# Kernel optimization log

Hardware: AMD Instinct MI355X
Metric: run time of the kernel (lower is better)

Reference implementation:

```python
import jax, jax.numpy as jnp
import numpy as np
import math

# hyperparams matching init_kwargs
GAMMA_S = 0.8
GAMMA_U = 0.8
RHO_I = 0.1
RHO_T = 0.1
EPS = 1e-10
TAU_MIN = 0.005
TAU_MAX = 1.0
TAU_INIT = 0.07
GRAD_CLIP = 5.0
ETA_INIT = 0.01
ETA_MIN = 0.0001
N_STATE = 2900000
BSZ = 4096
DIM = 1024


def setup_inputs() -> dict:
    key = jax.random.key(0)
    k1, k2 = jax.random.split(key)
    imf = jax.random.normal(k1, (BSZ, DIM), jnp.float32)
    imf = imf / jnp.linalg.norm(imf, axis=1, keepdims=True)
    txf = jax.random.normal(k2, (BSZ, DIM), jnp.float32)
    txf = txf / jnp.linalg.norm(txf, axis=1, keepdims=True)
    return {
        "image_features": imf,
        "text_features": txf,
        "s_I": jnp.zeros((N_STATE,), jnp.float32),
        "s_T": jnp.zeros((N_STATE,), jnp.float32),
        "tau_I": jnp.full((N_STATE,), TAU_INIT, jnp.float32),
        "tau_T": jnp.full((N_STATE,), TAU_INIT, jnp.float32),
        "u_I": jnp.zeros((N_STATE,), jnp.float32),
        "u_T": jnp.zeros((N_STATE,), jnp.float32),
        "b_I": jnp.zeros((N_STATE,), jnp.float32),
        "b_T": jnp.zeros((N_STATE,), jnp.float32),
        "image_ids": jnp.arange(BSZ, dtype=jnp.int32),
        "text_ids": jnp.arange(BSZ, dtype=jnp.int32),
        "epoch": 5,
        "max_epoch": 30,
    }


def reference(image_features, text_features, s_I, s_T, tau_I, tau_T,
              u_I, u_T, b_I, b_T, image_ids, text_ids, epoch, max_epoch):
    B = image_features.shape[0]
    sim = jnp.einsum('id,jd->ij', image_features, text_features)  # [B,B]
    diag_sim = jnp.diagonal(sim)                                  # [B]

    tau_image = tau_I[image_ids]  # [B]
    tau_text = tau_T[text_ids]    # [B]

    image_diffs = sim - diag_sim[:, None]
    text_diffs = sim - diag_sim[None, :]
    # .detach() in torch -> stop_gradient
    idt = jax.lax.stop_gradient(image_diffs / tau_image[:, None])
    tdt = jax.lax.stop_gradient(text_diffs / tau_text[None, :])

    # max-trick state b_I / b_T: running row/col max per sample id
    old_b_I = b_I[image_ids]
    new_b_I = jnp.maximum(jnp.max(idt, axis=1), old_b_I)  # [B]
    old_b_T = b_T[text_ids]
    new_b_T = jnp.maximum(jnp.max(tdt, axis=0), old_b_T)  # [B]

    exp_image_diffs = jnp.exp(idt - new_b_I[:, None])
    exp_text_diffs = jnp.exp(tdt - new_b_T[None, :])
    g_I = jnp.sum(exp_image_diffs, axis=1, keepdims=True) / (B - 1)  # [B,1]
    g_T = jnp.sum(exp_text_diffs, axis=0, keepdims=True) / (B - 1)   # [1,B]

    # moving-average s state (compute_last=False, last_g_* = None path)
    s_I_new = (1.0 - GAMMA_S) * s_I[image_ids] * jnp.exp(old_b_I - new_b_I) + GAMMA_S * g_I[:, 0]
    s_T_new = (1.0 - GAMMA_S) * s_T[text_ids] * jnp.exp(old_b_T - new_b_T) + GAMMA_S * g_T[0, :]
    s_I_b = s_I_new[:, None]  # same shape as g_I
    s_T_b = s_T_new[None, :]  # same shape as g_T

    weights_image = exp_image_diffs / (s_I_b + EPS)
    weights_text = exp_text_diffs / (s_T_b + EPS)

    image_loss = jnp.sum(weights_image * image_diffs, axis=1, keepdims=True) / (B - 1)
    text_loss = jnp.sum(weights_text * text_diffs, axis=0, keepdims=True) / (B - 1)
    total_loss = image_loss.mean() + text_loss.mean()

    grad_tau_image = (jnp.log(s_I_b) + new_b_I[:, None] + RHO_I
                      - jnp.sum(weights_image * idt, axis=1, keepdims=True) / (B - 1))
    grad_tau_text = (jnp.log(s_T_b) + new_b_T[None, :] + RHO_T
                     - jnp.sum(weights_text * tdt, axis=0, keepdims=True) / (B - 1))

    u_I_new = (1.0 - GAMMA_U) * u_I[image_ids] + GAMMA_U * jnp.clip(grad_tau_image[:, 0], -GRAD_CLIP, GRAD_CLIP)
    u_T_new = (1.0 - GAMMA_U) * u_T[text_ids] + GAMMA_U * jnp.clip(grad_tau_text[0, :], -GRAD_CLIP, GRAD_CLIP)

    eta_cur = ETA_MIN + (ETA_INIT - ETA_MIN) * math.cos(math.pi * (epoch / max_epoch) / 2)
    tau_I_new = jnp.clip(tau_image - eta_cur * u_I_new, TAU_MIN, TAU_MAX)
    tau_T_new = jnp.clip(tau_text - eta_cur * u_T_new, TAU_MIN, TAU_MAX)

    # scattered state writes (the module's in-place buffer updates)
    b_I_out = b_I.at[image_ids].set(new_b_I)
    b_T_out = b_T.at[text_ids].set(new_b_T)
    s_I_out = s_I.at[image_ids].set(s_I_new)
    s_T_out = s_T.at[text_ids].set(s_T_new)
    u_I_out = u_I.at[image_ids].set(u_I_new)
    u_T_out = u_T.at[text_ids].set(u_T_new)
    tau_I_out = tau_I.at[image_ids].set(tau_I_new)
    tau_T_out = tau_T.at[text_ids].set(tau_T_new)

    avg_image_tau = tau_image.mean()
    avg_text_tau = tau_text.mean()

    return (g_I, g_T, grad_tau_image, grad_tau_text, total_loss,
            avg_image_tau, avg_text_tau,
            s_I_out, s_T_out, u_I_out, u_T_out,
            b_I_out, b_T_out, tau_I_out, tau_T_out)
```

## Files before the change

kernel.cpp:

```cpp
#include <hip/hip_runtime.h>
#include <math.h>

#define BSZ 4096
#define DIM 1024
#define NST 2900000

constexpr float GAMMA_S   = 0.8f;
constexpr float GAMMA_U   = 0.8f;
constexpr float RHO_I_C   = 0.1f;
constexpr float RHO_T_C   = 0.1f;
constexpr float C_EPS     = 1e-10f;
constexpr float TAU_MIN_C = 0.005f;
constexpr float TAU_MAX_C = 1.0f;
constexpr float GCLIP     = 5.0f;
constexpr float ETA_INIT_C = 0.01f;
constexpr float ETA_MIN_C  = 1e-4f;
constexpr float PI_F       = 3.14159265358979323846f;

typedef __bf16 bf16x8 __attribute__((ext_vector_type(8)));
typedef float  f32x4  __attribute__((ext_vector_type(4)));

__device__ __forceinline__ unsigned short f2bf(float f) {
    unsigned int u = __float_as_uint(f);
    u += 0x7fffu + ((u >> 16) & 1u);
    return (unsigned short)(u >> 16);
}
__device__ __forceinline__ float bf2f(unsigned short s) {
    return __uint_as_float(((unsigned int)s) << 16);
}

__global__ __launch_bounds__(256) void conv_diag(const float* __restrict__ imf,
                                                 const float* __restrict__ txf,
                                                 unsigned short* __restrict__ abf,
                                                 unsigned short* __restrict__ bbf,
                                                 const float* __restrict__ tau_I,
                                                 const float* __restrict__ tau_T,
                                                 const float* __restrict__ b_I,
                                                 const float* __restrict__ b_T,
                                                 const int* __restrict__ iid,
                                                 const int* __restrict__ tid_,
                                                 float* diag, float* tauIg, float* tauTg,
                                                 float* obI, float* obT,
                                                 float* __restrict__ scal) {
    if (blockIdx.x == 0 && threadIdx.x < 3) scal[threadIdx.x] = 0.f;
    const int w  = threadIdx.x >> 6;
    const int ln = threadIdx.x & 63;
    const int i  = blockIdx.x * 4 + w;
    float dot = 0.f;
#pragma unroll
    for (int k = 0; k < 4; ++k) {
        const int off = i * DIM + k * 256 + ln * 4;
        float4 a = *(const float4*)&imf[off];
        float4 b = *(const float4*)&txf[off];
        ushort4 ra, rb;
        ra.x = f2bf(a.x); ra.y = f2bf(a.y); ra.z = f2bf(a.z); ra.w = f2bf(a.w);
        rb.x = f2bf(b.x); rb.y = f2bf(b.y); rb.z = f2bf(b.z); rb.w = f2bf(b.w);
        *(ushort4*)&abf[off] = ra;
        *(ushort4*)&bbf[off] = rb;
        dot += bf2f(ra.x) * bf2f(rb.x) + bf2f(ra.y) * bf2f(rb.y) +
               bf2f(ra.z) * bf2f(rb.z) + bf2f(ra.w) * bf2f(rb.w);
    }
#pragma unroll
    for (int m = 32; m; m >>= 1) dot += __shfl_xor(dot, m);
    if (ln == 0) {
        diag[i] = dot;
        const int id = iid[i];
        tauIg[i] = tau_I[id];
        obI[i]   = b_I[id];
        const int td = tid_[i];
        tauTg[i] = tau_T[td];
        obT[i]   = b_T[td];
    }
}

__device__ __forceinline__ void async16(const void* g, void* l) {
    __builtin_amdgcn_global_load_lds(
        (const __attribute__((address_space(1))) void*)g,
        (__attribute__((address_space(3))) void*)l, 16, 0, 0);
}

__global__ __launch_bounds__(256) void gemm_fused(const unsigned short* __restrict__ A,
                                                  const unsigned short* __restrict__ B,
                                                  const float* __restrict__ diag,
                                                  const float* __restrict__ tauIg,
                                                  const float* __restrict__ tauTg,
                                                  float* __restrict__ rpM,
                                                  float* __restrict__ rpE,
                                                  float* __restrict__ rpV,
                                                  float* __restrict__ cpM,
                                                  float* __restrict__ cpE,
                                                  float* __restrict__ cpV,
                                                  const float* __restrict__ s_I,
                                                  const float* __restrict__ s_T,
                                                  const float* __restrict__ u_I,
                                                  const float* __restrict__ u_T,
                                                  const float* __restrict__ b_I,
                                                  const float* __restrict__ b_T,
                                                  const float* __restrict__ tau_I,
                                                  const float* __restrict__ tau_T,
                                                  float* __restrict__ outbase) {
    __shared__ unsigned short As[128 * 32];
    __shared__ unsigned short Bs[128 * 32];

    const int tid = threadIdx.x;
    const int gid = ((blockIdx.x >> 4) << 3) | (blockIdx.x & 7);

    if ((blockIdx.x >> 3) & 1) {
        const size_t idx = (size_t)gid * 256 + tid;
        const size_t stride = (size_t)1024 * 256;
        const size_t NV = (NST - 1) / 4;
        const float* srcs[8] = {s_I, s_T, u_I, u_T, b_I, b_T, tau_I, tau_T};
#pragma unroll
        for (int a = 0; a < 8; ++a) {
            const float* s = srcs[a];
            float* d = outbase + (size_t)a * NST;
            for (size_t cidx = idx; cidx < NV; cidx += stride) {
                const size_t e = 1 + 4 * cidx;
                float4 v = make_float4(s[e], s[e + 1], s[e + 2], s[e + 3]);
                *(float4*)&d[e] = v;
            }
            if (idx == 0) d[0] = s[0];
            if (idx < 3)  d[NST - 3 + idx] = s[NST - 3 + idx];
        }
        return;
    }

    const int bjIdx = gid & 31, biIdx = gid >> 5;
    const int bi = biIdx * 128;
    const int bj = bjIdx * 128;
    const int lane = tid & 63;
    const int wave = tid >> 6;
    const int m_base = (wave >> 1) * 64;
    const int n_base = (wave & 1) * 64;

    const int c0 = tid, c1 = tid + 256;
    const int r0 = c0 >> 2, kg0 = ((c0 & 3) ^ ((r0 >> 1) & 3)) * 8;
    const int r1 = c1 >> 2, kg1 = ((c1 & 3) ^ ((r1 >> 1) & 3)) * 8;

    f32x4 acc[4][4];
#pragma unroll
    for (int m = 0; m < 4; ++m)
#pragma unroll
        for (int n = 0; n < 4; ++n)
            acc[m][n] = (f32x4){0.f, 0.f, 0.f, 0.f};

    const int mrow = lane & 15;
    const int q    = lane >> 4;

    for (int k0 = 0; k0 < DIM; k0 += 32) {
        __syncthreads();
        async16(&A[(size_t)(bi + r0) * DIM + k0 + kg0], &As[c0 * 8]);
        async16(&A[(size_t)(bi + r1) * DIM + k0 + kg1], &As[c1 * 8]);
        async16(&B[(size_t)(bj + r0) * DIM + k0 + kg0], &Bs[c0 * 8]);
        async16(&B[(size_t)(bj + r1) * DIM + k0 + kg1], &Bs[c1 * 8]);
        __syncthreads();

        bf16x8 af[4], bfr[4];
#pragma unroll
        for (int t = 0; t < 4; ++t) {
            const int rlA = m_base + t * 16 + mrow;
            const int rlB = n_base + t * 16 + mrow;
            af[t]  = *(const bf16x8*)&As[rlA * 32 + (q ^ ((rlA >> 1) & 3)) * 8];
            bfr[t] = *(const bf16x8*)&Bs[rlB * 32 + (q ^ ((rlB >> 1) & 3)) * 8];
        }
#pragma unroll
        for (int mt = 0; mt < 4; ++mt)
#pragma unroll
            for (int nt = 0; nt < 4; ++nt)
                acc[mt][nt] = __builtin_amdgcn_mfma_f32_16x16x32_bf16(
                    af[mt], bfr[nt], acc[mt][nt], 0, 0, 0);
    }

    __syncthreads();
    float* prm = (float*)Bs;
    if (tid < 128) {
        prm[tid]       = diag[bi + tid];
        prm[128 + tid] = 1.0f / tauIg[bi + tid];
        prm[256 + tid] = diag[bj + tid];
        prm[384 + tid] = 1.0f / tauTg[bj + tid];
    }
    __syncthreads();

    float* red = (float*)As;
    const int rowq = (lane >> 4) * 4;

#pragma unroll
    for (int mt = 0; mt < 4; ++mt)
#pragma unroll
        for (int r = 0; r < 4; ++r) {
            const int row_l = m_base + mt * 16 + rowq + r;
            const float dgr = prm[row_l];
            const float itr = prm[128 + row_l];
            float v0 = (acc[mt][0][r] - dgr) * itr;
            float v1 = (acc[mt][1][r] - dgr) * itr;
            float v2 = (acc[mt][2][r] - dgr) * itr;
            float v3 = (acc[mt][3][r] - dgr) * itr;
            float m = fmaxf(fmaxf(v0, v1), fmaxf(v2, v3));
#pragma unroll
            for (int x = 1; x <= 8; x <<= 1) m = fmaxf(m, __shfl_xor(m, x));
            const float e0 = __expf(v0 - m), e1 = __expf(v1 - m);
            const float e2 = __expf(v2 - m), e3 = __expf(v3 - m);
            float se = e0 + e1 + e2 + e3;
            float sv = e0 * v0 + e1 * v1 + e2 * v2 + e3 * v3;
#pragma unroll
            for (int x = 1; x <= 8; x <<= 1) {
                se += __shfl_xor(se, x);
                sv += __shfl_xor(sv, x);
            }
            if ((lane & 15) == 0) {
                const int idx = wave * 64 + mt * 16 + rowq + r;
                red[idx] = m; red[256 + idx] = se; red[512 + idx] = sv;
            }
        }

#pragma unroll
    for (int nt = 0; nt < 4; ++nt) {
        const int col_l = n_base + nt * 16 + (lane & 15);
        const float dgc = prm[256 + col_l];
        const float itc = prm[384 + col_l];
        float m = -INFINITY;
#pragma unroll
        for (int mt = 0; mt < 4; ++mt)
#pragma unroll
            for (int r = 0; r < 4; ++r)
                m = fmaxf(m, (acc[mt][nt][r] - dgc) * itc);
        m = fmaxf(m, __shfl_xor(m, 16));
        m = fmaxf(m, __shfl_xor(m, 32));
        float se = 0.f, sv = 0.f;
#pragma unroll
        for (int mt = 0; mt < 4; ++mt)
#pragma unroll
            for (int r = 0; r < 4; ++r) {
                const float v = (acc[mt][nt][r] - dgc) * itc;
                const float e = __expf(v - m);
                se += e; sv += e * v;
            }
        se += __shfl_xor(se, 16); se += __shfl_xor(se, 32);
        sv += __shfl_xor(sv, 16); sv += __shfl_xor(sv, 32);
        if (lane < 16) {
            const int idx = wave * 64 + nt * 16 + lane;
            red[768 + idx] = m; red[1024 + idx] = se; red[1280 + idx] = sv;
        }
    }
    __syncthreads();

    if (tid < 128) {
        const int rg = tid, li = rg & 63;
        const int w0 = (rg >> 6) * 2, w1 = w0 + 1;
        const float mA = red[w0 * 64 + li], mB = red[w1 * 64 + li];
        const float M = fmaxf(mA, mB);
        const float fA = __expf(mA - M), fB = __expf(mB - M);
        const size_t o = (size_t)bjIdx * BSZ + bi + rg;
        rpM[o] = M;
        rpE[o] = red[256 + w0 * 64 + li] * fA + red[256 + w1 * 64 + li] * fB;
        rpV[o] = red[512 + w0 * 64 + li] * fA + red[512 + w1 * 64 + li] * fB;
    } else {
        const int cg = tid - 128, li = cg & 63;
        const int w0 = cg >> 6, w1 = w0 + 2;
        const float mA = red[768 + w0 * 64 + li], mB = red[768 + w1 * 64 + li];
        const float M = fmaxf(mA, mB);
        const float fA = __expf(mA - M), fB = __expf(mB - M);
        const size_t o = (size_t)biIdx * BSZ + bj + cg;
        cpM[o] = M;
        cpE[o] = red[1024 + w0 * 64 + li] * fA + red[1024 + w1 * 64 + li] * fB;
        cpV[o] = red[1280 + w0 * 64 + li] * fA + red[1280 + w1 * 64 + li] * fB;
    }
}

__global__ __launch_bounds__(256) void finalize(const float* __restrict__ s_I,
                                                const float* __restrict__ s_T,
                                                const float* __restrict__ u_I,
                                                const float* __restrict__ u_T,
                                                const int* __restrict__ iid,
                                                const int* __restrict__ tid_,
                                                const int* __restrict__ epoch,
                                                const int* __restrict__ maxep,
                                                const float* __restrict__ tauIg,
                                                const float* __restrict__ tauTg,
                                                const float* __restrict__ obI,
                                                const float* __restrict__ obT,
                                                const float* __restrict__ rpM,
                                                const float* __restrict__ rpE,
                                                const float* __restrict__ rpV,
                                                const float* __restrict__ cpM,
                                                const float* __restrict__ cpE,
                                                const float* __restrict__ cpV,
                                                float* __restrict__ out) {
    const int i = blockIdx.x * 256 + threadIdx.x;

    const float eta = ETA_MIN_C + (ETA_INIT_C - ETA_MIN_C) *
                      cosf(0.5f * PI_F * ((float)epoch[0] / (float)maxep[0]));
    const float invBm1 = 1.0f / (float)(BSZ - 1);
    const float invB   = 1.0f / (float)BSZ;

    float* o_gI   = out;
    float* o_gT   = out + BSZ;
    float* o_gti  = out + 2 * BSZ;
    float* o_gtt  = out + 3 * BSZ;
    float* o_sI   = out + 4 * BSZ + 3;
    float* o_sT   = o_sI + NST;
    float* o_uI   = o_sT + NST;
    float* o_uT   = o_uI + NST;
    float* o_bI   = o_uT + NST;
    float* o_bT   = o_bI + NST;
    float* o_tauI = o_bT + NST;
    float* o_tauT = o_tauI + NST;

    float lossc, tI_B, tT_B;

    {
        const int id = iid[i];
        float mr = -INFINITY;
#pragma unroll
        for (int k = 0; k < 32; ++k) mr = fmaxf(mr, rpM[(size_t)k * BSZ + i]);
        const float tau = tauIg[i];
        const float ob = obI[i];
        const float nb = fmaxf(ob, mr);
        float se = 0.f, sv = 0.f;
#pragma unroll
        for (int k = 0; k < 32; ++k) {
            const float f = __expf(rpM[(size_t)k * BSZ + i] - nb);
            se += rpE[(size_t)k * BSZ + i] * f;
            sv += rpV[(size_t)k * BSZ + i] * f;
        }
        const float g = se * invBm1;
        const float s_new = (1.f - GAMMA_S) * s_I[id] * __expf(ob - nb) + GAMMA_S * g;
        const float W = sv * invBm1 / (s_new + C_EPS);
        const float grad = logf(s_new) + nb + RHO_I_C - W;
        lossc = tau * W;
        tI_B  = tau * invB;
        const float gc = fminf(fmaxf(grad, -GCLIP), GCLIP);
        const float u_new = (1.f - GAMMA_U) * u_I[id] + GAMMA_U * gc;
        const float tau_new = fminf(fmaxf(tau - eta * u_new, TAU_MIN_C), TAU_MAX_C);
        o_gI[i] = g;
        o_gti[i] = grad;
        o_sI[id] = s_new;
        o_uI[id] = u_new;
        o_bI[id] = nb;
        o_tauI[id] = tau_new;
    }
    {
        const int id = tid_[i];
        float mc = -INFINITY;
#pragma unroll
        for (int k = 0; k < 32; ++k) mc = fmaxf(mc, cpM[(size_t)k * BSZ + i]);
        const float tau = tauTg[i];
        const float ob = obT[i];
        const float nb = fmaxf(ob, mc);
        float se = 0.f, sv = 0.f;
#pragma unroll
        for (int k = 0; k < 32; ++k) {
            const float f = __expf(cpM[(size_t)k * BSZ + i] - nb);
            se += cpE[(size_t)k * BSZ + i] * f;
            sv += cpV[(size_t)k * BSZ + i] * f;
        }
        const float g = se * invBm1;
        const float s_new = (1.f - GAMMA_S) * s_T[id] * __expf(ob - nb) + GAMMA_S * g;
        const float W = sv * invBm1 / (s_new + C_EPS);
        const float grad = logf(s_new) + nb + RHO_T_C - W;
        lossc += tau * W;
        tT_B   = tau * invB;
        const float gc = fminf(fmaxf(grad, -GCLIP), GCLIP);
        const float u_new = (1.f - GAMMA_U) * u_T[id] + GAMMA_U * gc;
        const float tau_new = fminf(fmaxf(tau - eta * u_new, TAU_MIN_C), TAU_MAX_C);
        o_gT[i] = g;
        o_gtt[i] = grad;
        o_sT[id] = s_new;
        o_uT[id] = u_new;
        o_bT[id] = nb;
        o_tauT[id] = tau_new;
    }

    float v0 = lossc * invB, v1 = tI_B, v2 = tT_B;
#pragma unroll
    for (int o = 32; o; o >>= 1) {
        v0 += __shfl_down(v0, o);
        v1 += __shfl_down(v1, o);
        v2 += __shfl_down(v2, o);
    }
    __shared__ float lds[4][3];
    const int wv = threadIdx.x >> 6, ln = threadIdx.x & 63;
    if (ln == 0) { lds[wv][0] = v0; lds[wv][1] = v1; lds[wv][2] = v2; }
    __syncthreads();
    if (threadIdx.x == 0) {
        atomicAdd(&out[4 * BSZ + 0], lds[0][0] + lds[1][0] + lds[2][0] + lds[3][0]);
        atomicAdd(&out[4 * BSZ + 1], lds[0][1] + lds[1][1] + lds[2][1] + lds[3][1]);
        atomicAdd(&out[4 * BSZ + 2], lds[0][2] + lds[1][2] + lds[2][2] + lds[3][2]);
    }
}

extern "C" void kernel_launch(void* const* d_in, const int* in_sizes, int n_in,
                              void* d_out, int out_size, void* d_ws, size_t ws_size,
                              hipStream_t stream) {
    const float* imf   = (const float*)d_in[0];
    const float* txf   = (const float*)d_in[1];
    const float* s_I   = (const float*)d_in[2];
    const float* s_T   = (const float*)d_in[3];
    const float* tau_I = (const float*)d_in[4];
    const float* tau_T = (const float*)d_in[5];
    const float* u_I   = (const float*)d_in[6];
    const float* u_T   = (const float*)d_in[7];
    const float* b_I   = (const float*)d_in[8];
    const float* b_T   = (const float*)d_in[9];
    const int* iid     = (const int*)d_in[10];
    const int* tid_    = (const int*)d_in[11];
    const int* epoch   = (const int*)d_in[12];
    const int* maxep   = (const int*)d_in[13];

    float* out = (float*)d_out;
    float* ws  = (float*)d_ws;

    float* diag  = ws + 0 * BSZ;
    float* tauIg = ws + 1 * BSZ;
    float* tauTg = ws + 2 * BSZ;
    float* obI   = ws + 3 * BSZ;
    float* obT   = ws + 4 * BSZ;
    float* rpM   = ws + 5 * BSZ;
    float* rpE   = rpM + (size_t)32 * BSZ;
    float* rpV   = rpE + (size_t)32 * BSZ;
    float* cpM   = rpV + (size_t)32 * BSZ;
    float* cpE   = cpM + (size_t)32 * BSZ;
    float* cpV   = cpE + (size_t)32 * BSZ;
    unsigned short* abf = (unsigned short*)(cpV + (size_t)32 * BSZ);
    unsigned short* bbf = abf + (size_t)BSZ * DIM;

    conv_diag<<<BSZ / 4, 256, 0, stream>>>(imf, txf, abf, bbf, tau_I, tau_T, b_I, b_T,
                                           iid, tid_, diag, tauIg, tauTg, obI, obT,
                                           out + 4 * BSZ);
    gemm_fused<<<2048, 256, 0, stream>>>(abf, bbf, diag, tauIg, tauTg,
                                         rpM, rpE, rpV, cpM, cpE, cpV,
                                         s_I, s_T, u_I, u_T, b_I, b_T, tau_I, tau_T,
                                         out + 4 * BSZ + 3);
    finalize<<<BSZ / 256, 256, 0, stream>>>(s_I, s_T, u_I, u_T, iid, tid_, epoch, maxep,
                                            tauIg, tauTg, obI, obT,
                                            rpM, rpE, rpV, cpM, cpE, cpV, out);
}
```

Before: 283.4 us.

## Deepen GEMM K-tile to 64, vectorize state copy loads, parallelize finalize

The GEMM K-step grows from 32 to 64 with a new XOR swizzle over 8 chunks. This halves the number of barrier pairs per tile at the cost of doubled LDS. The state-copy loop now uses one aligned float4 load plus one scalar, replacing four scalar loads. The finalize kernel is split across 128 blocks, one per side and 64 rows, with the 32 partials reduced through LDS by 4 waves. This adds parallelism to a small tail kernel but spreads the loss reduction over more atomics.

```diff
diff --git a/kernel.cpp b/kernel.cpp
--- a/kernel.cpp
+++ b/kernel.cpp
@@ -99,8 +99,8 @@
                                                   const float* __restrict__ tau_I,
                                                   const float* __restrict__ tau_T,
                                                   float* __restrict__ outbase) {
-    __shared__ unsigned short As[128 * 32];
-    __shared__ unsigned short Bs[128 * 32];
+    __shared__ unsigned short As[128 * 64];
+    __shared__ unsigned short Bs[128 * 64];
 
     const int tid = threadIdx.x;
     const int gid = ((blockIdx.x >> 4) << 3) | (blockIdx.x & 7);
@@ -115,9 +115,9 @@
             const float* s = srcs[a];
             float* d = outbase + (size_t)a * NST;
             for (size_t cidx = idx; cidx < NV; cidx += stride) {
-                const size_t e = 1 + 4 * cidx;
-                float4 v = make_float4(s[e], s[e + 1], s[e + 2], s[e + 3]);
-                *(float4*)&d[e] = v;
+                const float4 f = *(const float4*)&s[4 * cidx];
+                const float nx = s[4 * cidx + 4];
+                *(float4*)&d[1 + 4 * cidx] = make_float4(f.y, f.z, f.w, nx);
             }
             if (idx == 0) d[0] = s[0];
             if (idx < 3)  d[NST - 3 + idx] = s[NST - 3 + idx];
@@ -133,10 +133,6 @@
     const int m_base = (wave >> 1) * 64;
     const int n_base = (wave & 1) * 64;
 
-    const int c0 = tid, c1 = tid + 256;
-    const int r0 = c0 >> 2, kg0 = ((c0 & 3) ^ ((r0 >> 1) & 3)) * 8;
-    const int r1 = c1 >> 2, kg1 = ((c1 & 3) ^ ((r1 >> 1) & 3)) * 8;
-
     f32x4 acc[4][4];
 #pragma unroll
     for (int m = 0; m < 4; ++m)
@@ -147,28 +143,36 @@
     const int mrow = lane & 15;
     const int q    = lane >> 4;
 
-    for (int k0 = 0; k0 < DIM; k0 += 32) {
+    for (int k0 = 0; k0 < DIM; k0 += 64) {
         __syncthreads();
-        async16(&A[(size_t)(bi + r0) * DIM + k0 + kg0], &As[c0 * 8]);
-        async16(&A[(size_t)(bi + r1) * DIM + k0 + kg1], &As[c1 * 8]);
-        async16(&B[(size_t)(bj + r0) * DIM + k0 + kg0], &Bs[c0 * 8]);
-        async16(&B[(size_t)(bj + r1) * DIM + k0 + kg1], &Bs[c1 * 8]);
+#pragma unroll
+        for (int j = 0; j < 4; ++j) {
+            const int c   = tid + j * 256;
+            const int row = c >> 3;
+            const int kk  = ((c & 7) ^ (row & 7)) << 3;
+            async16(&A[(size_t)(bi + row) * DIM + k0 + kk], &As[c * 8]);
+            async16(&B[(size_t)(bj + row) * DIM + k0 + kk], &Bs[c * 8]);
+        }
         __syncthreads();
-
-        bf16x8 af[4], bfr[4];
-#pragma unroll
-        for (int t = 0; t < 4; ++t) {
-            const int rlA = m_base + t * 16 + mrow;
-            const int rlB = n_base + t * 16 + mrow;
-            af[t]  = *(const bf16x8*)&As[rlA * 32 + (q ^ ((rlA >> 1) & 3)) * 8];
-            bfr[t] = *(const bf16x8*)&Bs[rlB * 32 + (q ^ ((rlB >> 1) & 3)) * 8];
-        }
-#pragma unroll
-        for (int mt = 0; mt < 4; ++mt)
-#pragma unroll
-            for (int nt = 0; nt < 4; ++nt)
-                acc[mt][nt] = __builtin_amdgcn_mfma_f32_16x16x32_bf16(
-                    af[mt], bfr[nt], acc[mt][nt], 0, 0, 0);
+#pragma unroll
+        for (int ks = 0; ks < 2; ++ks) {
+            bf16x8 af[4], bfr[4];
+#pragma unroll
+            for (int t = 0; t < 4; ++t) {
+                const int rlA = m_base + t * 16 + mrow;
+                const int rlB = n_base + t * 16 + mrow;
+                const int slA = (((ks << 2) + q) ^ (rlA & 7)) << 3;
+                const int slB = (((ks << 2) + q) ^ (rlB & 7)) << 3;
+                af[t]  = *(const bf16x8*)&As[rlA * 64 + slA];
+                bfr[t] = *(const bf16x8*)&Bs[rlB * 64 + slB];
+            }
+#pragma unroll
+            for (int mt = 0; mt < 4; ++mt)
+#pragma unroll
+                for (int nt = 0; nt < 4; ++nt)
+                    acc[mt][nt] = __builtin_amdgcn_mfma_f32_16x16x32_bf16(
+                        af[mt], bfr[nt], acc[mt][nt], 0, 0, 0);
+        }
     }
 
     __syncthreads();
@@ -286,106 +290,95 @@
                                                 const float* __restrict__ cpE,
                                                 const float* __restrict__ cpV,
                                                 float* __restrict__ out) {
-    const int i = blockIdx.x * 256 + threadIdx.x;
-
-    const float eta = ETA_MIN_C + (ETA_INIT_C - ETA_MIN_C) *
-                      cosf(0.5f * PI_F * ((float)epoch[0] / (float)maxep[0]));
-    const float invBm1 = 1.0f / (float)(BSZ - 1);
-    const float invB   = 1.0f / (float)BSZ;
-
-    float* o_gI   = out;
-    float* o_gT   = out + BSZ;
-    float* o_gti  = out + 2 * BSZ;
-    float* o_gtt  = out + 3 * BSZ;
-    float* o_sI   = out + 4 * BSZ + 3;
-    float* o_sT   = o_sI + NST;
-    float* o_uI   = o_sT + NST;
-    float* o_uT   = o_uI + NST;
-    float* o_bI   = o_uT + NST;
-    float* o_bT   = o_bI + NST;
-    float* o_tauI = o_bT + NST;
-    float* o_tauT = o_tauI + NST;
-
-    float lossc, tI_B, tT_B;
-
-    {
-        const int id = iid[i];
-        float mr = -INFINITY;
-#pragma unroll
-        for (int k = 0; k < 32; ++k) mr = fmaxf(mr, rpM[(size_t)k * BSZ + i]);
-        const float tau = tauIg[i];
-        const float ob = obI[i];
-        const float nb = fmaxf(ob, mr);
-        float se = 0.f, sv = 0.f;
-#pragma unroll
-        for (int k = 0; k < 32; ++k) {
-            const float f = __expf(rpM[(size_t)k * BSZ + i] - nb);
-            se += rpE[(size_t)k * BSZ + i] * f;
-            sv += rpV[(size_t)k * BSZ + i] * f;
-        }
-        const float g = se * invBm1;
-        const float s_new = (1.f - GAMMA_S) * s_I[id] * __expf(ob - nb) + GAMMA_S * g;
-        const float W = sv * invBm1 / (s_new + C_EPS);
-        const float grad = logf(s_new) + nb + RHO_I_C - W;
-        lossc = tau * W;
-        tI_B  = tau * invB;
-        const float gc = fminf(fmaxf(grad, -GCLIP), GCLIP);
-        const float u_new = (1.f - GAMMA_U) * u_I[id] + GAMMA_U * gc;
+    const int side = blockIdx.x & 1;
+    const int i0   = (blockIdx.x >> 1) * 64;
+    const int w    = threadIdx.x >> 6;
+    const int il   = threadIdx.x & 63;
+    const int i    = i0 + il;
+
+    const float* pM  = side ? cpM  : rpM;
+    const float* pE  = side ? cpE  : rpE;
+    const float* pV  = side ? cpV  : rpV;
+    const float* tg  = side ? tauTg : tauIg;
+    const float* obA = side ? obT  : obI;
+    const float* sA  = side ? s_T  : s_I;
+    const float* uA  = side ? u_T  : u_I;
+    const int*   ids = side ? tid_ : iid;
+    const float  rho = side ? RHO_T_C : RHO_I_C;
+
+    float M[8], E[8], V[8];
+#pragma unroll
+    for (int k = 0; k < 8; ++k) {
+        const size_t o = (size_t)(w * 8 + k) * BSZ + i;
+        M[k] = pM[o]; E[k] = pE[o]; V[k] = pV[o];
+    }
+    float pm = M[0];
+#pragma unroll
+    for (int k = 1; k < 8; ++k) pm = fmaxf(pm, M[k]);
+
+    __shared__ float lred[12][64];
+    lred[w][il] = pm;
+    __syncthreads();
+
+    const float ob = obA[i];
+    const float nb = fmaxf(fmaxf(fmaxf(lred[0][il], lred[1][il]),
+                                 fmaxf(lred[2][il], lred[3][il])), ob);
+    float se = 0.f, sv = 0.f;
+#pragma unroll
+    for (int k = 0; k < 8; ++k) {
+        const float f = __expf(M[k] - nb);
+        se += E[k] * f;
+        sv += V[k] * f;
+    }
+    lred[4 + w][il] = se;
+    lred[8 + w][il] = sv;
+    __syncthreads();
+
+    if (w == 0) {
+        const float eta = ETA_MIN_C + (ETA_INIT_C - ETA_MIN_C) *
+                          cosf(0.5f * PI_F * ((float)epoch[0] / (float)maxep[0]));
+        const float invBm1 = 1.0f / (float)(BSZ - 1);
+        const float invB   = 1.0f / (float)BSZ;
+
+        const int   id  = ids[i];
+        const float tau = tg[i];
+        const float seT = (lred[4][il] + lred[5][il]) + (lred[6][il] + lred[7][il]);
+        const float svT = (lred[8][il] + lred[9][il]) + (lred[10][il] + lred[11][il]);
+
+        const float g     = seT * invBm1;
+        const float s_new = (1.f - GAMMA_S) * sA[id] * __expf(ob - nb) + GAMMA_S * g;
+        const float W     = svT * invBm1 / (s_new + C_EPS);
+        const float grad  = logf(s_new) + nb + rho - W;
+        const float gc    = fminf(fmaxf(grad, -GCLIP), GCLIP);
+        const float u_new = (1.f - GAMMA_U) * uA[id] + GAMMA_U * gc;
         const float tau_new = fminf(fmaxf(tau - eta * u_new, TAU_MIN_C), TAU_MAX_C);
-        o_gI[i] = g;
-        o_gti[i] = grad;
-        o_sI[id] = s_new;
-        o_uI[id] = u_new;
-        o_bI[id] = nb;
-        o_tauI[id] = tau_new;
-    }
-    {
-        const int id = tid_[i];
-        float mc = -INFINITY;
-#pragma unroll
-        for (int k = 0; k < 32; ++k) mc = fmaxf(mc, cpM[(size_t)k * BSZ + i]);
-        const float tau = tauTg[i];
-        const float ob = obT[i];
-        const float nb = fmaxf(ob, mc);
-        float se = 0.f, sv = 0.f;
-#pragma unroll
-        for (int k = 0; k < 32; ++k) {
-            const float f = __expf(cpM[(size_t)k * BSZ + i] - nb);
-            se += cpE[(size_t)k * BSZ + i] * f;
-            sv += cpV[(size_t)k * BSZ + i] * f;
-        }
-        const float g = se * invBm1;
-        const float s_new = (1.f - GAMMA_S) * s_T[id] * __expf(ob - nb) + GAMMA_S * g;
-        const float W = sv * invBm1 / (s_new + C_EPS);
-        const float grad = logf(s_new) + nb + RHO_T_C - W;
-        lossc += tau * W;
-        tT_B   = tau * invB;
-        const float gc = fminf(fmaxf(grad, -GCLIP), GCLIP);
-        const float u_new = (1.f - GAMMA_U) * u_T[id] + GAMMA_U * gc;
-        const float tau_new = fminf(fmaxf(tau - eta * u_new, TAU_MIN_C), TAU_MAX_C);
-        o_gT[i] = g;
-        o_gtt[i] = grad;
-        o_sT[id] = s_new;
-        o_uT[id] = u_new;
-        o_bT[id] = nb;
-        o_tauT[id] = tau_new;
-    }
-
-    float v0 = lossc * invB, v1 = tI_B, v2 = tT_B;
-#pragma unroll
-    for (int o = 32; o; o >>= 1) {
-        v0 += __shfl_down(v0, o);
-        v1 += __shfl_down(v1, o);
-        v2 += __shfl_down(v2, o);
-    }
-    __shared__ float lds[4][3];
-    const int wv = threadIdx.x >> 6, ln = threadIdx.x & 63;
-    if (ln == 0) { lds[wv][0] = v0; lds[wv][1] = v1; lds[wv][2] = v2; }
-    __syncthreads();
-    if (threadIdx.x == 0) {
-        atomicAdd(&out[4 * BSZ + 0], lds[0][0] + lds[1][0] + lds[2][0] + lds[3][0]);
-        atomicAdd(&out[4 * BSZ + 1], lds[0][1] + lds[1][1] + lds[2][1] + lds[3][1]);
-        atomicAdd(&out[4 * BSZ + 2], lds[0][2] + lds[1][2] + lds[2][2] + lds[3][2]);
+
+        float* o_g   = out + side * BSZ;
+        float* o_gt  = out + (2 + side) * BSZ;
+        float* stb   = out + 4 * BSZ + 3;
+        float* o_s   = stb + (size_t)side * NST;
+        float* o_u   = stb + (size_t)(2 + side) * NST;
+        float* o_b   = stb + (size_t)(4 + side) * NST;
+        float* o_t   = stb + (size_t)(6 + side) * NST;
+
+        o_g[i]  = g;
+        o_gt[i] = grad;
+        o_s[id] = s_new;
+        o_u[id] = u_new;
+        o_b[id] = nb;
+        o_t[id] = tau_new;
+
+        float v0 = tau * W * invB;
+        float v1 = tau * invB;
+#pragma unroll
+        for (int o2 = 32; o2; o2 >>= 1) {
+            v0 += __shfl_down(v0, o2);
+            v1 += __shfl_down(v1, o2);
+        }
+        if (il == 0) {
+            atomicAdd(&out[4 * BSZ + 0], v0);
+            atomicAdd(&out[4 * BSZ + 1 + side], v1);
+        }
     }
 }
 
@@ -431,7 +424,7 @@
                                          rpM, rpE, rpV, cpM, cpE, cpV,
                                          s_I, s_T, u_I, u_T, b_I, b_T, tau_I, tau_T,
                                          out + 4 * BSZ + 3);
-    finalize<<<BSZ / 256, 256, 0, stream>>>(s_I, s_T, u_I, u_T, iid, tid_, epoch, maxep,
-                                            tauIg, tauTg, obI, obT,
-                                            rpM, rpE, rpV, cpM, cpE, cpV, out);
-}
+    finalize<<<128, 256, 0, stream>>>(s_I, s_T, u_I, u_T, iid, tid_, epoch, maxep,
+                                      tauIg, tauTg, obI, obT,
+                                      rpM, rpE, rpV, cpM, cpE, cpV, out);
+}
```

After: 305.4 us. 7.8% more time.
